# Kernel tuning notes

Hardware: AMD Instinct MI355X
Metric: run time of the kernel (lower is better)

The kernel has to match this reference:

```python
import jax, jax.numpy as jnp
import numpy as np
import math

B, N, C = 8, 4096, 768
H = 12
DH = C // H
M = 256
LN_EPS = 1e-5


def setup_inputs() -> dict:
    key = jax.random.key(0)
    ks = jax.random.split(key, 7)
    x = jax.random.normal(ks[0], (B, N, C), dtype=jnp.float32)
    # torch Linear weight [out,in]; store transposed for y = x @ W
    W_qkv = jax.random.normal(ks[1], (C, 3 * C), dtype=jnp.float32) * (1.0 / math.sqrt(C))
    W_proj = jax.random.normal(ks[2], (C, C), dtype=jnp.float32) * (1.0 / math.sqrt(C))
    b_proj = jnp.zeros((C,), dtype=jnp.float32)
    gamma = jnp.ones((C,), dtype=jnp.float32)
    beta = jnp.zeros((C,), dtype=jnp.float32)
    random_features = jax.random.normal(ks[3], (M, DH), dtype=jnp.float32) / math.sqrt(DH)
    return {"x": x, "W_qkv": W_qkv, "W_proj": W_proj, "b_proj": b_proj,
            "gamma": gamma, "beta": beta, "random_features": random_features}


def _phi(t, random_features):
    # t: [B, H, N, DH] -> [B, H, N, M]; phi(x) = exp(w·x - ||x||^2/2) / sqrt(M)
    norm_sq = 0.5 * jnp.sum(t * t, axis=-1, keepdims=True)
    proj = jnp.einsum('bhnd,md->bhnm', t, random_features)
    return jnp.exp(proj - norm_sq) * (1.0 / math.sqrt(M))


def reference(x, W_qkv, W_proj, b_proj, gamma, beta, random_features):
    b, n, c = x.shape
    qkv = (x @ W_qkv).reshape(b, n, 3, H, DH)
    qkv = jnp.transpose(qkv, (2, 0, 3, 1, 4))  # [3, B, H, N, DH]
    q, k, v = qkv[0], qkv[1], qkv[2]

    q_p = _phi(q, random_features)  # [B,H,N,M]
    k_p = _phi(k, random_features)  # [B,H,N,M]

    kv = jnp.einsum('bhnm,bhnd->bhmd', k_p, v)       # [B,H,M,DH]
    out = jnp.einsum('bhnm,bhmd->bhnd', q_p, kv)     # [B,H,N,DH]

    k_sum = jnp.sum(k_p, axis=2)                      # [B,H,M]
    normalizer = jnp.einsum('bhnm,bhm->bhn', q_p, k_sum)[..., None]
    out = out / (normalizer + 1e-6)

    x_attn = jnp.transpose(out, (0, 2, 1, 3)).reshape(b, n, c)
    x_attn = x_attn @ W_proj + b_proj
    # dropout is identity in eval / p=0

    y = x + x_attn
    mu = jnp.mean(y, axis=-1, keepdims=True)
    var = jnp.mean(jnp.square(y - mu), axis=-1, keepdims=True)
    return (y - mu) * jax.lax.rsqrt(var + LN_EPS) * gamma + beta
```

## Files before the change

### kernel.cpp

```cpp
#include <hip/hip_runtime.h>
#include <hip/hip_fp16.h>


#define LOG2E 1.44269504088896340736f

typedef _Float16 half8 __attribute__((ext_vector_type(8)));
typedef _Float16 half4_t __attribute__((ext_vector_type(4)));
typedef _Float16 half2_t __attribute__((ext_vector_type(2)));
typedef float f32x4 __attribute__((ext_vector_type(4)));

#if __has_builtin(__builtin_amdgcn_fdot2)
#define FDOT2(a, b, c) __builtin_amdgcn_fdot2((a), (b), (c), false)
#else
#define FDOT2(a, b, c) \
  ((float)(a)[0] * (float)(b)[0] + ((float)(a)[1] * (float)(b)[1] + (c)))
#endif

static __device__ __forceinline__ half2_t pk2(float a, float b) {
#if __has_builtin(__builtin_amdgcn_cvt_pkrtz)
  return __builtin_bit_cast(half2_t, __builtin_amdgcn_cvt_pkrtz(a, b));
#else
  half2_t r; r[0] = (_Float16)a; r[1] = (_Float16)b; return r;
#endif
}

__device__ __forceinline__ void glds16(const _Float16* g, _Float16* s) {
  __builtin_amdgcn_global_load_lds(
      (const __attribute__((address_space(1))) void*)g,
      (__attribute__((address_space(3))) unsigned int*)s,
      16, 0, 0);
}


__global__ __launch_bounds__(256)
void prep(const float* __restrict__ x, const float* __restrict__ Wqkv,
          const float* __restrict__ Wproj, const float* __restrict__ rfm,
          _Float16* __restrict__ x_h, _Float16* __restrict__ wqkvT,
          _Float16* __restrict__ wprojT, _Float16* __restrict__ rfh) {
  __shared__ _Float16 T[64][72];
  const int bid = blockIdx.x;
  if (bid < 24576) {
    long i = ((long)bid * 256 + threadIdx.x) * 4;
    float4 v = *(const float4*)(x + i);
    half4_t h;
    h[0] = (_Float16)v.x; h[1] = (_Float16)v.y; h[2] = (_Float16)v.z; h[3] = (_Float16)v.w;
    *(half4_t*)(x_h + i) = h;
    return;
  }
  int tb = bid - 24576;
  if (tb < 576) {
    const float* src; _Float16* dst; int Csrc, r0, c0;
    if (tb < 432) {
      r0 = (tb / 36) * 64; c0 = (tb % 36) * 64; src = Wqkv; dst = wqkvT; Csrc = 2304;
    } else {
      int t2 = tb - 432;
      r0 = (t2 / 12) * 64; c0 = (t2 % 12) * 64; src = Wproj; dst = wprojT; Csrc = 768;
    }
    const int ri = threadIdx.x >> 4;
    const int ci = (threadIdx.x & 15) * 4;
#pragma unroll
    for (int rr = 0; rr < 4; ++rr) {
      float4 v = *(const float4*)(src + (long)(r0 + ri * 4 + rr) * Csrc + c0 + ci);
      T[ci + 0][ri * 4 + rr] = (_Float16)v.x;
      T[ci + 1][ri * 4 + rr] = (_Float16)v.y;
      T[ci + 2][ri * 4 + rr] = (_Float16)v.z;
      T[ci + 3][ri * 4 + rr] = (_Float16)v.w;
    }
    __syncthreads();
    const int wi = threadIdx.x >> 3;
    const int wj = (threadIdx.x & 7) * 8;
#pragma unroll
    for (int ww = 0; ww < 2; ++ww) {
      const int row = wi * 2 + ww;
      half8 h = *(const half8*)(&T[row][wj]);
      *(half8*)(dst + (long)(c0 + row) * 768 + r0 + wj) = h;
    }
  } else {
    int idx = (tb - 576) * 256 + threadIdx.x;
    if (idx < 16384) rfh[idx] = (_Float16)rfm[idx];
  }
}


__device__ __forceinline__ void stage_unit(const _Float16* __restrict__ G, int grow0,
                                           int kcol, _Float16* lds, int w, int l) {
#pragma unroll
  for (int j = 0; j < 2; ++j) {
    const int ci = w + j * 8;
    const int row = ci * 8 + (l >> 3);
    const int col8 = (l & 7) ^ (row & 7);
    glds16(G + (long)(grow0 + row) * 768 + kcol + col8 * 8, lds + ci * 512);
  }
}

static __device__ __forceinline__ half8 ldsw(const _Float16* buf, int r, int sl) {
  return *(const half8*)(buf + r * 64 + ((sl ^ (r & 7)) << 3));
}

__global__ __launch_bounds__(512)
void gemm_qkv(const _Float16* __restrict__ W, const _Float16* __restrict__ X,
              _Float16* __restrict__ qh, _Float16* __restrict__ kh,
              _Float16* __restrict__ vT,
              float* __restrict__ nsqLq, float* __restrict__ nsqLk) {
  __shared__ __align__(16) _Float16 SMEM[65536];
  _Float16* As = SMEM;
  _Float16* Bs = SMEM + 32768;
  const int tid = threadIdx.x;
  const int w = tid >> 6, l = tid & 63;
  const int lr = l & 15, kg = l >> 4;
  const int wr = w >> 2, wc = w & 3;

  const int bid = blockIdx.x;
  const int wg = (bid & 7) * 144 + (bid >> 3);
  const int m0 = (wg % 9) * 256;
  const int n0 = (wg / 9) * 256;

  stage_unit(W, m0,       0,  As,         w, l);
  stage_unit(X, n0,       0,  Bs,         w, l);
  stage_unit(X, n0 + 128, 0,  Bs + 8192,  w, l);
  stage_unit(W, m0 + 128, 0,  As + 8192,  w, l);
  stage_unit(W, m0,       64, As + 16384, w, l);
  stage_unit(X, n0,       64, Bs + 16384, w, l);
  stage_unit(X, n0 + 128, 64, Bs + 24576, w, l);
  asm volatile("s_waitcnt vmcnt(6)" ::: "memory");
  __builtin_amdgcn_s_barrier();

  f32x4 acc[8][4];
#pragma unroll
  for (int t = 0; t < 8; ++t)
#pragma unroll
    for (int u = 0; u < 4; ++u) acc[t][u] = (f32x4){0.f, 0.f, 0.f, 0.f};

  for (int kt = 0; kt < 12; ++kt) {
    const int c = kt & 1, o = c ^ 1;
    const _Float16* Ac = As + c * 16384;
    const _Float16* Bc = Bs + c * 16384;
    half8 aR[4][2], bR0[2][2], bR1[2][2];

#pragma unroll
    for (int i = 0; i < 4; ++i) {
      const int r = wr * 16 + i * 32 + lr;
      aR[i][0] = ldsw(Ac, r, kg);
      aR[i][1] = ldsw(Ac, r, 4 + kg);
    }
#pragma unroll
    for (int j = 0; j < 2; ++j) {
      const int r = wc * 16 + j * 64 + lr;
      bR0[j][0] = ldsw(Bc, r, kg);
      bR0[j][1] = ldsw(Bc, r, 4 + kg);
    }
    if (kt + 1 < 12)
      stage_unit(W, m0 + 128, (kt + 1) * 64, As + o * 16384 + 8192, w, l);
    __builtin_amdgcn_s_barrier();
    __builtin_amdgcn_s_setprio(1);
#pragma unroll
    for (int ks = 0; ks < 2; ++ks)
#pragma unroll
      for (int i = 0; i < 4; ++i)
#pragma unroll
        for (int j = 0; j < 2; ++j)
          acc[i][j] = __builtin_amdgcn_mfma_f32_16x16x32_f16(aR[i][ks], bR0[j][ks],
                                                             acc[i][j], 0, 0, 0);
    __builtin_amdgcn_s_setprio(0);
    __builtin_amdgcn_s_barrier();

#pragma unroll
    for (int j = 0; j < 2; ++j) {
      const int r = 128 + wc * 16 + j * 64 + lr;
      bR1[j][0] = ldsw(Bc, r, kg);
      bR1[j][1] = ldsw(Bc, r, 4 + kg);
    }
    if (kt + 2 < 12)
      stage_unit(W, m0, (kt + 2) * 64, As + c * 16384, w, l);
    __builtin_amdgcn_s_barrier();
    __builtin_amdgcn_s_setprio(1);
#pragma unroll
    for (int ks = 0; ks < 2; ++ks)
#pragma unroll
      for (int i = 0; i < 4; ++i)
#pragma unroll
        for (int j = 0; j < 2; ++j)
          acc[i][2 + j] = __builtin_amdgcn_mfma_f32_16x16x32_f16(aR[i][ks], bR1[j][ks],
                                                                 acc[i][2 + j], 0, 0, 0);
    __builtin_amdgcn_s_setprio(0);
    __builtin_amdgcn_s_barrier();

#pragma unroll
    for (int i = 0; i < 4; ++i) {
      const int r = 128 + wr * 16 + i * 32 + lr;
      aR[i][0] = ldsw(Ac, r, kg);
      aR[i][1] = ldsw(Ac, r, 4 + kg);
    }
    if (kt + 2 < 12)
      stage_unit(X, n0, (kt + 2) * 64, Bs + c * 16384, w, l);
    __builtin_amdgcn_s_barrier();
    __builtin_amdgcn_s_setprio(1);
#pragma unroll
    for (int ks = 0; ks < 2; ++ks)
#pragma unroll
      for (int i = 0; i < 4; ++i)
#pragma unroll
        for (int j = 0; j < 2; ++j)
          acc[4 + i][2 + j] = __builtin_amdgcn_mfma_f32_16x16x32_f16(aR[i][ks], bR1[j][ks],
                                                                     acc[4 + i][2 + j], 0, 0, 0);
    __builtin_amdgcn_s_setprio(0);
    __builtin_amdgcn_s_barrier();

    if (kt + 2 < 12)
      stage_unit(X, n0 + 128, (kt + 2) * 64, Bs + c * 16384 + 8192, w, l);
    if (kt < 10)
      asm volatile("s_waitcnt vmcnt(6)" ::: "memory");
    else
      asm volatile("s_waitcnt vmcnt(0)" ::: "memory");
    __builtin_amdgcn_s_barrier();
    __builtin_amdgcn_s_setprio(1);
#pragma unroll
    for (int ks = 0; ks < 2; ++ks)
#pragma unroll
      for (int i = 0; i < 4; ++i)
#pragma unroll
        for (int j = 0; j < 2; ++j)
          acc[4 + i][j] = __builtin_amdgcn_mfma_f32_16x16x32_f16(aR[i][ks], bR0[j][ks],
                                                                 acc[4 + i][j], 0, 0, 0);
    __builtin_amdgcn_s_setprio(0);
    __builtin_amdgcn_s_barrier();
  }

  const int which = (m0 >= 1536) ? 2 : ((m0 >= 768) ? 1 : 0);
  const int hbase = (m0 - which * 768) >> 6;
  const int b_ = n0 >> 12;
  const int nb = n0 & 4095;

  if (which < 2) {
    _Float16* dst = which ? kh : qh;
    float* nd = which ? nsqLk : nsqLq;
#pragma unroll
    for (int t = 0; t < 8; ++t) {
      const int m_ = wr * 16 + t * 32 + kg * 4;
#pragma unroll
      for (int u = 0; u < 4; ++u) {
        const int n_ = wc * 16 + u * 64 + lr;
        half2_t h01 = pk2(acc[t][u][0], acc[t][u][1]);
        half2_t h23 = pk2(acc[t][u][2], acc[t][u][3]);
        half4_t p4; p4[0] = h01[0]; p4[1] = h01[1]; p4[2] = h23[0]; p4[3] = h23[1];
        *(half4_t*)((char*)SMEM + n_ * 512 + (((m_ >> 3) ^ (n_ & 7)) << 4) +
                    (m_ & 4) * 2) = p4;
      }
    }
    __syncthreads();
    const int h2 = w >> 1;
    const int jj = l & 7;
    const long bhout = (long)(b_ * 12 + hbase + h2);
#pragma unroll
    for (int i = 0; i < 16; ++i) {
      const int n_ = (w & 1) * 128 + i * 8 + (l >> 3);
      const int phys = (h2 * 8 + jj) ^ (n_ & 7);
      half8 v = *(const half8*)((const char*)SMEM + n_ * 512 + phys * 16);
      *(half8*)(dst + (bhout * 4096 + nb + n_) * 64 + jj * 8) = v;
      float s = 0.f;
#pragma unroll
      for (int e = 0; e < 8; ++e) { float f = (float)v[e]; s += f * f; }
      s += __shfl_xor(s, 1);
      s += __shfl_xor(s, 2);
      s += __shfl_xor(s, 4);
      if (jj == 0) nd[bhout * 4096 + nb + n_] = 0.5f * s * LOG2E + 4.0f;
    }
  } else {
#pragma unroll
    for (int t = 0; t < 8; ++t) {
#pragma unroll
      for (int u = 0; u < 4; ++u) {
        const int n_ = wc * 16 + u * 64 + lr;
#pragma unroll
        for (int r = 0; r < 4; ++r) {
          const int m_ = wr * 16 + t * 32 + kg * 4 + r;
          *(_Float16*)((char*)SMEM + m_ * 512 + ((((n_ >> 3)) ^ (m_ & 7)) << 4) +
                       (n_ & 7) * 2) = (_Float16)acc[t][u][r];
        }
      }
    }
    __syncthreads();
#pragma unroll
    for (int i = 0; i < 16; ++i) {
      const int m_ = w * 32 + i * 2 + (l >> 5);
      const int c = l & 31;
      half8 v = *(const half8*)((const char*)SMEM + m_ * 512 + ((c ^ (m_ & 7)) << 4));
      const int h2 = m_ >> 6, d = m_ & 63;
      *(half8*)(vT + ((long)(b_ * 12 + hbase + h2) * 64 + d) * 4096 + nb + c * 8) = v;
    }
  }
}


__global__ __launch_bounds__(256)
void gemm_proj(const _Float16* __restrict__ A, const _Float16* __restrict__ BT,
               float* __restrict__ Co, const float* __restrict__ bias,
               const float* __restrict__ resid) {
  __shared__ __align__(16) _Float16 As[128 * 32];
  __shared__ __align__(16) _Float16 Bs[128 * 32];
  const int tid = threadIdx.x;
  const int w = tid >> 6, l = tid & 63;
  const int lr = l & 15, kg = l >> 4;
  const int m0 = blockIdx.y * 128;
  const int n0 = blockIdx.x * 128;
  const int wm = (w >> 1) * 64, wn = (w & 1) * 64;

  const _Float16* gA = A + (long)(m0 + w * 32 + (l >> 2)) * 768 + (l & 3) * 8;
  const _Float16* gB = BT + (long)(n0 + w * 32 + (l >> 2)) * 768 + (l & 3) * 8;
  _Float16* sA = As + (w * 32) * 32;
  _Float16* sB = Bs + (w * 32) * 32;

  f32x4 acc[4][4];
#pragma unroll
  for (int t = 0; t < 4; ++t)
#pragma unroll
    for (int u = 0; u < 4; ++u) acc[t][u] = (f32x4){0.f, 0.f, 0.f, 0.f};

  for (int kc = 0; kc < 24; ++kc) {
    __syncthreads();
    glds16(gA, sA);
    glds16(gA + 16 * 768, sA + 16 * 32);
    glds16(gB, sB);
    glds16(gB + 16 * 768, sB + 16 * 32);
    gA += 32; gB += 32;
    __syncthreads();

    half8 af[4], bf[4];
#pragma unroll
    for (int t = 0; t < 4; ++t)
      af[t] = *(const half8*)(As + (wm + t * 16 + lr) * 32 + kg * 8);
#pragma unroll
    for (int u = 0; u < 4; ++u)
      bf[u] = *(const half8*)(Bs + (wn + u * 16 + lr) * 32 + kg * 8);
#pragma unroll
    for (int t = 0; t < 4; ++t)
#pragma unroll
      for (int u = 0; u < 4; ++u)
        acc[t][u] = __builtin_amdgcn_mfma_f32_16x16x32_f16(af[t], bf[u], acc[t][u], 0, 0, 0);
  }

#pragma unroll
  for (int u = 0; u < 4; ++u) {
    const int col = n0 + wn + u * 16 + lr;
    const float bv = bias[col];
#pragma unroll
    for (int t = 0; t < 4; ++t) {
      const int row = m0 + wm + t * 16 + kg * 4;
#pragma unroll
      for (int r = 0; r < 4; ++r) {
        long idx = (long)(row + r) * 768 + col;
        Co[idx] = acc[t][u][r] + bv + resid[idx];
      }
    }
  }
}


__global__ __launch_bounds__(256)
void kv_fused(const _Float16* __restrict__ kh, const _Float16* __restrict__ vT,
              const _Float16* __restrict__ rfh, const float* __restrict__ nsqLk,
              _Float16* __restrict__ kvpart, float* __restrict__ kspart) {
  __shared__ __align__(16) _Float16 P[256 * 72];
  const int chunk = blockIdx.x, bh = blockIdx.y;
  const int tid = threadIdx.x, w = tid >> 6, l = tid & 63;
  const int lr = l & 15, kg = l >> 4;
  const long khbase = (long)bh * 4096 * 64;
  const long vtbase = (long)bh * 64 * 4096;
  const half2_t ONES = {(_Float16)1.f, (_Float16)1.f};

  half8 rf[4][2];
#pragma unroll
  for (int u = 0; u < 4; ++u)
#pragma unroll
    for (int ks = 0; ks < 2; ++ks)
      rf[u][ks] = *(const half8*)(rfh + (w * 64 + u * 16 + lr) * 64 + ks * 32 + kg * 8);

  f32x4 kvacc[4][4];
#pragma unroll
  for (int mt = 0; mt < 4; ++mt)
#pragma unroll
    for (int dt = 0; dt < 4; ++dt) kvacc[mt][dt] = (f32x4){0.f, 0.f, 0.f, 0.f};
  float ksacc[4] = {0.f, 0.f, 0.f, 0.f};

  for (int t8 = 0; t8 < 8; ++t8) {
    const int nt = chunk * 512 + t8 * 64;

    half8 af[4][2];
#pragma unroll
    for (int tt = 0; tt < 4; ++tt)
#pragma unroll
      for (int ks = 0; ks < 2; ++ks)
        af[tt][ks] = *(const half8*)(kh + khbase + (long)(nt + tt * 16 + lr) * 64 +
                                     ks * 32 + kg * 8);

    f32x4 sacc[4][4];
#pragma unroll
    for (int tt = 0; tt < 4; ++tt)
#pragma unroll
      for (int u = 0; u < 4; ++u) sacc[tt][u] = (f32x4){0.f, 0.f, 0.f, 0.f};
#pragma unroll
    for (int ks = 0; ks < 2; ++ks)
#pragma unroll
      for (int tt = 0; tt < 4; ++tt)
#pragma unroll
        for (int u = 0; u < 4; ++u)
          sacc[tt][u] = __builtin_amdgcn_mfma_f32_16x16x32_f16(af[tt][ks], rf[u][ks],
                                                               sacc[tt][u], 0, 0, 0);
    float4 nsq4[4];
#pragma unroll
    for (int tt = 0; tt < 4; ++tt)
      nsq4[tt] = *(const float4*)(nsqLk + (long)bh * 4096 + nt + tt * 16 + kg * 4);
#pragma unroll
    for (int tt = 0; tt < 4; ++tt)
#pragma unroll
      for (int u = 0; u < 4; ++u) {
        float e0 = exp2f(sacc[tt][u][0] * LOG2E - nsq4[tt].x);
        float e1 = exp2f(sacc[tt][u][1] * LOG2E - nsq4[tt].y);
        float e2 = exp2f(sacc[tt][u][2] * LOG2E - nsq4[tt].z);
        float e3 = exp2f(sacc[tt][u][3] * LOG2E - nsq4[tt].w);
        half2_t h01 = pk2(e0, e1), h23 = pk2(e2, e3);
        half4_t p4; p4[0] = h01[0]; p4[1] = h01[1]; p4[2] = h23[0]; p4[3] = h23[1];
        *(half4_t*)(P + (w * 64 + u * 16 + lr) * 72 + tt * 16 + kg * 4) = p4;
      }

#pragma unroll
    for (int ks = 0; ks < 2; ++ks) {
      half8 pa[4], bv[4];
#pragma unroll
      for (int mt = 0; mt < 4; ++mt)
        pa[mt] = *(const half8*)(P + (w * 64 + mt * 16 + lr) * 72 + ks * 32 + kg * 8);
#pragma unroll
      for (int dt = 0; dt < 4; ++dt)
        bv[dt] = *(const half8*)(vT + vtbase + (long)(dt * 16 + lr) * 4096 + nt +
                                 ks * 32 + kg * 8);
#pragma unroll
      for (int mt = 0; mt < 4; ++mt)
#pragma unroll
        for (int dt = 0; dt < 4; ++dt)
          kvacc[mt][dt] = __builtin_amdgcn_mfma_f32_16x16x32_f16(pa[mt], bv[dt],
                                                                 kvacc[mt][dt], 0, 0, 0);
#pragma unroll
      for (int mt = 0; mt < 4; ++mt) {
        const half2_t* pp = (const half2_t*)&pa[mt];
#pragma unroll
        for (int p = 0; p < 4; ++p) ksacc[mt] = FDOT2(pp[p], ONES, ksacc[mt]);
      }
    }
  }

#pragma unroll
  for (int mt = 0; mt < 4; ++mt) {
    float v = ksacc[mt];
    v += __shfl_xor(v, 16);
    v += __shfl_xor(v, 32);
    if (l < 16) kspart[((bh * 8 + chunk) << 8) + w * 64 + mt * 16 + l] = v;
  }
#pragma unroll
  for (int mt = 0; mt < 4; ++mt)
#pragma unroll
    for (int dt = 0; dt < 4; ++dt)
#pragma unroll
      for (int r = 0; r < 4; ++r)
        kvpart[(((long)(bh * 8 + chunk) * 256) + w * 64 + mt * 16 + kg * 4 + r) * 64 +
               dt * 16 + lr] = (_Float16)kvacc[mt][dt][r];
}


__global__ __launch_bounds__(256)
void reduce_all(const _Float16* __restrict__ kvpart, const float* __restrict__ kspart,
                _Float16* __restrict__ kvT, _Float16* __restrict__ ksumh) {
  if (blockIdx.x < 6144) {
    long i = (long)blockIdx.x * 256 + threadIdx.x;
    const int bh = (int)(i >> 14);
    const int rem = (int)(i & 16383);
    const int m = rem >> 6, d = rem & 63;
    float s = 0.f;
#pragma unroll
    for (int c = 0; c < 8; ++c)
      s += (float)kvpart[(((long)bh * 8 + c) * 256 + m) * 64 + d];
    kvT[(long)bh * 16384 + d * 256 + m] = (_Float16)s;
  } else {
    int i = (blockIdx.x - 6144) * 256 + threadIdx.x;
    int bh = i >> 8, m = i & 255;
    float s = 0.f;
#pragma unroll
    for (int c = 0; c < 8; ++c) s += kspart[((bh * 8 + c) << 8) + m];
    ksumh[i] = (_Float16)s;
  }
}


__global__ __launch_bounds__(256)
void attn_fused(const _Float16* __restrict__ qh, const _Float16* __restrict__ rfh,
                const float* __restrict__ nsqLq, const _Float16* __restrict__ kvT,
                const _Float16* __restrict__ ksumh, _Float16* __restrict__ attn) {
  __shared__ __align__(16) _Float16 KV[64 * 264];
  __shared__ __align__(16) _Float16 KS[256];
  __shared__ __align__(16) _Float16 P[64 * 264];
  __shared__ __align__(16) float NS[64];
  const int chunk = blockIdx.x, bh = blockIdx.y;
  const int b = bh / 12, h = bh % 12;
  const int tid = threadIdx.x, w = tid >> 6, l = tid & 63;
  const int lr = l & 15, kg = l >> 4;

  {
    const int d = tid >> 2, mb = (tid & 3) * 64;
#pragma unroll
    for (int j = 0; j < 8; ++j)
      *(half8*)(KV + d * 264 + mb + j * 8) =
          *(const half8*)(kvT + (long)bh * 16384 + d * 256 + mb + j * 8);
    if (tid < 32) *(half8*)(KS + tid * 8) = *(const half8*)(ksumh + bh * 256 + tid * 8);
  }

  half8 rf[4][2];
#pragma unroll
  for (int mt = 0; mt < 4; ++mt)
#pragma unroll
    for (int ks = 0; ks < 2; ++ks)
      rf[mt][ks] = *(const half8*)(rfh + (w * 64 + mt * 16 + lr) * 64 + ks * 32 + kg * 8);

  for (int t8 = 0; t8 < 4; ++t8) {
    const int nt = chunk * 256 + t8 * 64;
    __syncthreads();

    half8 bq[4][2];
#pragma unroll
    for (int tt = 0; tt < 4; ++tt)
#pragma unroll
      for (int ks = 0; ks < 2; ++ks)
        bq[tt][ks] = *(const half8*)(qh + ((long)bh * 4096 + nt + tt * 16 + lr) * 64 +
                                     ks * 32 + kg * 8);

    f32x4 sacc[4][4];
#pragma unroll
    for (int mt = 0; mt < 4; ++mt)
#pragma unroll
      for (int tt = 0; tt < 4; ++tt) sacc[mt][tt] = (f32x4){0.f, 0.f, 0.f, 0.f};
#pragma unroll
    for (int ks = 0; ks < 2; ++ks)
#pragma unroll
      for (int mt = 0; mt < 4; ++mt)
#pragma unroll
        for (int tt = 0; tt < 4; ++tt)
          sacc[mt][tt] = __builtin_amdgcn_mfma_f32_16x16x32_f16(rf[mt][ks], bq[tt][ks],
                                                                sacc[mt][tt], 0, 0, 0);
    float nsqv[4];
#pragma unroll
    for (int tt = 0; tt < 4; ++tt)
      nsqv[tt] = nsqLq[(long)bh * 4096 + nt + tt * 16 + lr];
#pragma unroll
    for (int mt = 0; mt < 4; ++mt)
#pragma unroll
      for (int tt = 0; tt < 4; ++tt) {
        float e0 = exp2f(sacc[mt][tt][0] * LOG2E - nsqv[tt]);
        float e1 = exp2f(sacc[mt][tt][1] * LOG2E - nsqv[tt]);
        float e2 = exp2f(sacc[mt][tt][2] * LOG2E - nsqv[tt]);
        float e3 = exp2f(sacc[mt][tt][3] * LOG2E - nsqv[tt]);
        half2_t h01 = pk2(e0, e1), h23 = pk2(e2, e3);
        half4_t p4; p4[0] = h01[0]; p4[1] = h01[1]; p4[2] = h23[0]; p4[3] = h23[1];
        *(half4_t*)(P + (tt * 16 + lr) * 264 + w * 64 + mt * 16 + kg * 4) = p4;
      }
    __syncthreads();

    f32x4 oacc[4];
#pragma unroll
    for (int u = 0; u < 4; ++u) oacc[u] = (f32x4){0.f, 0.f, 0.f, 0.f};
    float nacc = 0.f;
#pragma unroll
    for (int ks = 0; ks < 8; ++ks) {
      half8 ap = *(const half8*)(P + (w * 16 + lr) * 264 + ks * 32 + kg * 8);
      half8 kv8 = *(const half8*)(KS + ks * 32 + kg * 8);
      const half2_t* a2 = (const half2_t*)&ap;
      const half2_t* k2 = (const half2_t*)&kv8;
#pragma unroll
      for (int p = 0; p < 4; ++p) nacc = FDOT2(a2[p], k2[p], nacc);
#pragma unroll
      for (int u = 0; u < 4; ++u) {
        half8 bkv = *(const half8*)(KV + (u * 16 + lr) * 264 + ks * 32 + kg * 8);
        oacc[u] = __builtin_amdgcn_mfma_f32_16x16x32_f16(ap, bkv, oacc[u], 0, 0, 0);
      }
    }
    nacc += __shfl_xor(nacc, 16);
    nacc += __shfl_xor(nacc, 32);
    if (l < 16) NS[w * 16 + l] = nacc;
    f32x4 n4 = *(const f32x4*)(NS + w * 16 + kg * 4);
    float inv[4];
#pragma unroll
    for (int r = 0; r < 4; ++r) inv[r] = 1.f / (n4[r] + 1e-6f);
#pragma unroll
    for (int u = 0; u < 4; ++u)
#pragma unroll
      for (int r = 0; r < 4; ++r)
        attn[((long)b * 4096 + nt + w * 16 + kg * 4 + r) * 768 + h * 64 + u * 16 + lr] =
            (_Float16)(oacc[u][r] * inv[r]);
  }
}


__global__ __launch_bounds__(256)
void ln_kernel(const float* __restrict__ y, const float* __restrict__ gamma,
               const float* __restrict__ beta, float* __restrict__ outp) {
  const int wv = threadIdx.x >> 6, l = threadIdx.x & 63;
  const long row = (long)blockIdx.x * 4 + wv;
  const float* yr = y + row * 768;
  float v[12];
  float s = 0.f;
#pragma unroll
  for (int j = 0; j < 12; ++j) { v[j] = yr[l + j * 64]; s += v[j]; }
#pragma unroll
  for (int off = 32; off; off >>= 1) s += __shfl_xor(s, off);
  const float mu = s * (1.f / 768.f);
  float vs = 0.f;
#pragma unroll
  for (int j = 0; j < 12; ++j) { float d = v[j] - mu; vs += d * d; }
#pragma unroll
  for (int off = 32; off; off >>= 1) vs += __shfl_xor(vs, off);
  const float rstd = rsqrtf(vs * (1.f / 768.f) + 1e-5f);
  float* orp = outp + row * 768;
#pragma unroll
  for (int j = 0; j < 12; ++j)
    orp[l + j * 64] = (v[j] - mu) * rstd * gamma[l + j * 64] + beta[l + j * 64];
}


extern "C" void kernel_launch(void* const* d_in, const int* in_sizes, int n_in,
                              void* d_out, int out_size, void* d_ws, size_t ws_size,
                              hipStream_t stream) {
  const float* x = (const float*)d_in[0];
  const float* Wqkv = (const float*)d_in[1];
  const float* Wproj = (const float*)d_in[2];
  const float* bproj = (const float*)d_in[3];
  const float* gamma = (const float*)d_in[4];
  const float* beta = (const float*)d_in[5];
  const float* rfm = (const float*)d_in[6];

  char* ws = (char*)d_ws;
  size_t off = 0;
  auto alloc = [&](size_t bytes) -> void* {
    void* p = ws + off;
    off += (bytes + 255) & ~(size_t)255;
    return p;
  };
  char* regionA = (char*)alloc(50331648ULL);
  _Float16* x_h = (_Float16*)regionA;
  _Float16* kvpart = (_Float16*)regionA;
  _Float16* attn = (_Float16*)regionA;

  _Float16* wqkvT = (_Float16*)alloc(1769472ULL * 2);
  _Float16* wprojT = (_Float16*)alloc(589824ULL * 2);
  _Float16* rfh = (_Float16*)alloc(16384ULL * 2);
  _Float16* qh = (_Float16*)alloc(25165824ULL * 2);
  _Float16* kh = (_Float16*)alloc(25165824ULL * 2);
  _Float16* vT = (_Float16*)alloc(25165824ULL * 2);
  float* nsqLq = (float*)alloc(393216ULL * 4);
  float* nsqLk = (float*)alloc(393216ULL * 4);
  float* kspart = (float*)alloc(96ULL * 8 * 256 * 4);
  _Float16* kvT = (_Float16*)alloc(96ULL * 16384 * 2);
  _Float16* ksumh = (_Float16*)alloc(96ULL * 256 * 2);

  float* y = (float*)d_out;

  prep<<<25216, 256, 0, stream>>>(x, Wqkv, Wproj, rfm, x_h, wqkvT, wprojT, rfh);
  gemm_qkv<<<1152, 512, 0, stream>>>(wqkvT, x_h, qh, kh, vT, nsqLq, nsqLk);
  kv_fused<<<dim3(8, 96), 256, 0, stream>>>(kh, vT, rfh, nsqLk, kvpart, kspart);
  reduce_all<<<6240, 256, 0, stream>>>(kvpart, kspart, kvT, ksumh);
  attn_fused<<<dim3(16, 96), 256, 0, stream>>>(qh, rfh, nsqLq, kvT, ksumh, attn);
  gemm_proj<<<dim3(6, 256), 256, 0, stream>>>(attn, wprojT, y, bproj, x);
  ln_kernel<<<8192, 256, 0, stream>>>(y, gamma, beta, y);
}
```

Measured before the change: 580.3 us.

## Fuse output projection GEMM with residual add and LayerNorm in one kernel

Replaces the tiled proj GEMM and the separate LayerNorm kernel with one kernel. Each 512-thread block computes 64 full rows of 768 columns, stages its A tile (96KB, XOR-swizzled) in shared memory, and reads B fragments straight from global memory. LayerNorm statistics are reduced in registers and shared memory, which removes the fp32 y round trip and one launch. In exchange it uses only 512 blocks with large LDS and high register use, reads weights uncached by LDS, and computes variance as E[x^2]-mu^2, which is less numerically stable.

```diff
diff --git a/kernel.cpp b/kernel.cpp
--- a/kernel.cpp
+++ b/kernel.cpp
@@ -292,67 +292,118 @@
 }
 
 
-__global__ __launch_bounds__(256)
-void gemm_proj(const _Float16* __restrict__ A, const _Float16* __restrict__ BT,
-               float* __restrict__ Co, const float* __restrict__ bias,
-               const float* __restrict__ resid) {
-  __shared__ __align__(16) _Float16 As[128 * 32];
-  __shared__ __align__(16) _Float16 Bs[128 * 32];
+__global__ __launch_bounds__(512)
+void proj_ln(const _Float16* __restrict__ A, const _Float16* __restrict__ BT,
+             const float* __restrict__ bias, const float* __restrict__ xres,
+             const float* __restrict__ gamma, const float* __restrict__ beta,
+             float* __restrict__ y) {
+  __shared__ __align__(16) _Float16 Asm[64 * 768];
+  __shared__ __align__(16) float lnS[64][8];
+  __shared__ __align__(16) float lnQ[64][8];
   const int tid = threadIdx.x;
   const int w = tid >> 6, l = tid & 63;
   const int lr = l & 15, kg = l >> 4;
-  const int m0 = blockIdx.y * 128;
-  const int n0 = blockIdx.x * 128;
-  const int wm = (w >> 1) * 64, wn = (w & 1) * 64;
-
-  const _Float16* gA = A + (long)(m0 + w * 32 + (l >> 2)) * 768 + (l & 3) * 8;
-  const _Float16* gB = BT + (long)(n0 + w * 32 + (l >> 2)) * 768 + (l & 3) * 8;
-  _Float16* sA = As + (w * 32) * 32;
-  _Float16* sB = Bs + (w * 32) * 32;
-
-  f32x4 acc[4][4];
-#pragma unroll
-  for (int t = 0; t < 4; ++t)
-#pragma unroll
-    for (int u = 0; u < 4; ++u) acc[t][u] = (f32x4){0.f, 0.f, 0.f, 0.f};
-
-  for (int kc = 0; kc < 24; ++kc) {
-    __syncthreads();
-    glds16(gA, sA);
-    glds16(gA + 16 * 768, sA + 16 * 32);
-    glds16(gB, sB);
-    glds16(gB + 16 * 768, sB + 16 * 32);
-    gA += 32; gB += 32;
-    __syncthreads();
-
-    half8 af[4], bf[4];
-#pragma unroll
-    for (int t = 0; t < 4; ++t)
-      af[t] = *(const half8*)(As + (wm + t * 16 + lr) * 32 + kg * 8);
-#pragma unroll
-    for (int u = 0; u < 4; ++u)
-      bf[u] = *(const half8*)(Bs + (wn + u * 16 + lr) * 32 + kg * 8);
-#pragma unroll
-    for (int t = 0; t < 4; ++t)
-#pragma unroll
-      for (int u = 0; u < 4; ++u)
-        acc[t][u] = __builtin_amdgcn_mfma_f32_16x16x32_f16(af[t], bf[u], acc[t][u], 0, 0, 0);
-  }
-
-#pragma unroll
-  for (int u = 0; u < 4; ++u) {
-    const int col = n0 + wn + u * 16 + lr;
-    const float bv = bias[col];
-#pragma unroll
-    for (int t = 0; t < 4; ++t) {
-      const int row = m0 + wm + t * 16 + kg * 4;
-#pragma unroll
-      for (int r = 0; r < 4; ++r) {
-        long idx = (long)(row + r) * 768 + col;
-        Co[idx] = acc[t][u][r] + bv + resid[idx];
-      }
-    }
-  }
+  const int m0 = blockIdx.x * 64;
+  const int ncol0 = w * 96;
+
+#pragma unroll
+  for (int i = 0; i < 12; ++i) {
+    const int sg = i * 512 + tid;
+    const int row = sg / 96;
+    const int p = sg - row * 96;
+    glds16(A + (long)(m0 + row) * 768 + ((p ^ (row & 7)) << 3), Asm + sg * 8);
+  }
+  asm volatile("s_waitcnt vmcnt(0)" ::: "memory");
+  __builtin_amdgcn_s_barrier();
+
+  f32x4 acc[4][6];
+#pragma unroll
+  for (int mf = 0; mf < 4; ++mf)
+#pragma unroll
+    for (int nf = 0; nf < 6; ++nf) acc[mf][nf] = (f32x4){0.f, 0.f, 0.f, 0.f};
+
+#pragma unroll 2
+  for (int kc = 0; kc < 12; ++kc) {
+    half8 bf[6][2];
+#pragma unroll
+    for (int nf = 0; nf < 6; ++nf)
+#pragma unroll
+      for (int ks = 0; ks < 2; ++ks)
+        bf[nf][ks] = *(const half8*)(BT + (long)(ncol0 + nf * 16 + lr) * 768 +
+                                     kc * 64 + ks * 32 + kg * 8);
+    half8 af[4][2];
+#pragma unroll
+    for (int mf = 0; mf < 4; ++mf) {
+      const int r = mf * 16 + lr;
+#pragma unroll
+      for (int ks = 0; ks < 2; ++ks)
+        af[mf][ks] = *(const half8*)(Asm + r * 768 +
+                                     (((kc * 8 + ks * 4 + kg) ^ (lr & 7)) << 3));
+    }
+#pragma unroll
+    for (int ks = 0; ks < 2; ++ks)
+#pragma unroll
+      for (int mf = 0; mf < 4; ++mf)
+#pragma unroll
+        for (int nf = 0; nf < 6; ++nf)
+          acc[mf][nf] = __builtin_amdgcn_mfma_f32_16x16x32_f16(af[mf][ks], bf[nf][ks],
+                                                               acc[mf][nf], 0, 0, 0);
+  }
+
+  float bv[6], gv[6], betv[6];
+#pragma unroll
+  for (int nf = 0; nf < 6; ++nf) {
+    const int col = ncol0 + nf * 16 + lr;
+    bv[nf] = bias[col]; gv[nf] = gamma[col]; betv[nf] = beta[col];
+  }
+#pragma unroll
+  for (int mf = 0; mf < 4; ++mf)
+#pragma unroll
+    for (int r = 0; r < 4; ++r) {
+      const int row = mf * 16 + kg * 4 + r;
+#pragma unroll
+      for (int nf = 0; nf < 6; ++nf)
+        acc[mf][nf][r] += bv[nf] + xres[(long)(m0 + row) * 768 + ncol0 + nf * 16 + lr];
+    }
+#pragma unroll
+  for (int mf = 0; mf < 4; ++mf)
+#pragma unroll
+    for (int r = 0; r < 4; ++r) {
+      float s = 0.f, q = 0.f;
+#pragma unroll
+      for (int nf = 0; nf < 6; ++nf) {
+        const float v = acc[mf][nf][r];
+        s += v; q += v * v;
+      }
+      s += __shfl_xor(s, 1); q += __shfl_xor(q, 1);
+      s += __shfl_xor(s, 2); q += __shfl_xor(q, 2);
+      s += __shfl_xor(s, 4); q += __shfl_xor(q, 4);
+      s += __shfl_xor(s, 8); q += __shfl_xor(q, 8);
+      if (lr == 0) {
+        const int row = mf * 16 + kg * 4 + r;
+        lnS[row][w] = s; lnQ[row][w] = q;
+      }
+    }
+  __syncthreads();
+#pragma unroll
+  for (int mf = 0; mf < 4; ++mf)
+#pragma unroll
+    for (int r = 0; r < 4; ++r) {
+      const int row = mf * 16 + kg * 4 + r;
+      f32x4 s0 = *(const f32x4*)&lnS[row][0];
+      f32x4 s1 = *(const f32x4*)&lnS[row][4];
+      f32x4 q0 = *(const f32x4*)&lnQ[row][0];
+      f32x4 q1 = *(const f32x4*)&lnQ[row][4];
+      const float s = s0[0] + s0[1] + s0[2] + s0[3] + s1[0] + s1[1] + s1[2] + s1[3];
+      const float q = q0[0] + q0[1] + q0[2] + q0[3] + q1[0] + q1[1] + q1[2] + q1[3];
+      const float mu = s * (1.f / 768.f);
+      const float var = q * (1.f / 768.f) - mu * mu;
+      const float rstd = rsqrtf(var + 1e-5f);
+#pragma unroll
+      for (int nf = 0; nf < 6; ++nf)
+        y[(long)(m0 + row) * 768 + ncol0 + nf * 16 + lr] =
+            (acc[mf][nf][r] - mu) * rstd * gv[nf] + betv[nf];
+    }
 }
 
 
@@ -597,32 +648,6 @@
 }
 
 
-__global__ __launch_bounds__(256)
-void ln_kernel(const float* __restrict__ y, const float* __restrict__ gamma,
-               const float* __restrict__ beta, float* __restrict__ outp) {
-  const int wv = threadIdx.x >> 6, l = threadIdx.x & 63;
-  const long row = (long)blockIdx.x * 4 + wv;
-  const float* yr = y + row * 768;
-  float v[12];
-  float s = 0.f;
-#pragma unroll
-  for (int j = 0; j < 12; ++j) { v[j] = yr[l + j * 64]; s += v[j]; }
-#pragma unroll
-  for (int off = 32; off; off >>= 1) s += __shfl_xor(s, off);
-  const float mu = s * (1.f / 768.f);
-  float vs = 0.f;
-#pragma unroll
-  for (int j = 0; j < 12; ++j) { float d = v[j] - mu; vs += d * d; }
-#pragma unroll
-  for (int off = 32; off; off >>= 1) vs += __shfl_xor(vs, off);
-  const float rstd = rsqrtf(vs * (1.f / 768.f) + 1e-5f);
-  float* orp = outp + row * 768;
-#pragma unroll
-  for (int j = 0; j < 12; ++j)
-    orp[l + j * 64] = (v[j] - mu) * rstd * gamma[l + j * 64] + beta[l + j * 64];
-}
-
-
 extern "C" void kernel_launch(void* const* d_in, const int* in_sizes, int n_in,
                               void* d_out, int out_size, void* d_ws, size_t ws_size,
                               hipStream_t stream) {
@@ -665,6 +690,5 @@
   kv_fused<<<dim3(8, 96), 256, 0, stream>>>(kh, vT, rfh, nsqLk, kvpart, kspart);
   reduce_all<<<6240, 256, 0, stream>>>(kvpart, kspart, kvT, ksumh);
   attn_fused<<<dim3(16, 96), 256, 0, stream>>>(qh, rfh, nsqLq, kvT, ksumh, attn);
-  gemm_proj<<<dim3(6, 256), 256, 0, stream>>>(attn, wprojT, y, bproj, x);
-  ln_kernel<<<8192, 256, 0, stream>>>(y, gamma, beta, y);
-}
+  proj_ln<<<512, 512, 0, stream>>>(attn, wprojT, bproj, x, gamma, beta, y);
+}
```

Measured after the change: 560.7 us. -3.4%, faster.
